# Kernel tuning notes

Hardware: AMD Instinct MI355X
Metric: run time of the kernel (lower is better)

The kernel has to match this reference:

```python
import jax, jax.numpy as jnp
import numpy as np

COMMITMENT_COST = 0.25
NUM_EMBEDDINGS = 512
EMBEDDING_DIM = 64


def setup_inputs() -> dict:
    key = jax.random.key(0)
    k1, k2 = jax.random.split(key)
    inputs = jax.random.normal(k1, (32, EMBEDDING_DIM, 64, 64), dtype=jnp.float32)  # NCHW
    embedding_weight = jax.random.normal(k2, (NUM_EMBEDDINGS, EMBEDDING_DIM), dtype=jnp.float32)
    return {"inputs": inputs, "embedding_weight": embedding_weight}


def reference(inputs, embedding_weight):
    # NCHW -> NHWC, flatten to [N, D]
    x = jnp.transpose(inputs, (0, 2, 3, 1))  # [B,H,W,D]
    input_shape = x.shape
    flat = x.reshape(-1, EMBEDDING_DIM)  # [N, D]

    distances = (jnp.sum(flat * flat, axis=1, keepdims=True)
                 + jnp.sum(embedding_weight * embedding_weight, axis=1)
                 - 2.0 * jnp.matmul(flat, embedding_weight.T))

    encoding_indices = jnp.argmin(distances, axis=1)  # [N]
    encodings = jax.nn.one_hot(encoding_indices, NUM_EMBEDDINGS, dtype=jnp.float32)  # [N, K]

    # quantized lookup (== encodings @ embedding_weight)
    quantized = jnp.take(embedding_weight, encoding_indices, axis=0).reshape(input_shape)

    # commitment loss (eval path; EMA buffer updates are a training-time side effect)
    encoder_loss = jnp.mean((jax.lax.stop_gradient(quantized) - x) ** 2)
    loss = COMMITMENT_COST * encoder_loss

    # straight-through estimator
    quantized_st = x + jax.lax.stop_gradient(quantized - x)

    avg_probs = jnp.mean(encodings, axis=0)
    perplexity = jnp.exp(-jnp.sum(avg_probs * jnp.log(avg_probs + 1e-10)))

    return (loss, jnp.transpose(quantized_st, (0, 3, 1, 2)), perplexity, encodings)
```

## Files before the change

### kernel.cpp

```cpp
#include <hip/hip_runtime.h>
#include <math.h>

#define N_ROWS 131072
#define D 64
#define K 512
#define BLK 512
#define ROWS_PER_BLK 512
#define GRID (N_ROWS / ROWS_PER_BLK)
#define MARGIN 4e-3f


typedef __attribute__((ext_vector_type(8))) _Float16 f16x8;
typedef __attribute__((ext_vector_type(4))) float    f32x4;

#define MFMA(a, b, c) __builtin_amdgcn_mfma_f32_16x16x32_f16((a), (b), (c), 0, 0, 0)

#define OFF_EH   0
#define OFF_EL   65536
#define OFF_XH   0
#define OFF_XL   65536
#define OFF_E2   131072
#define OFF_IDX  133120
#define OFF_REF  135168
#define OFF_HIST 137216
#define OFF_RED  139264
#define ARENA_SZ 143360

__global__ __launch_bounds__(256) void vq_e2_kernel(
    const float* __restrict__ emb, float* __restrict__ e2)
{
    int k = blockIdx.x * blockDim.x + threadIdx.x;
    if (k < K) {
        const float* e = emb + k * D;
        float s = 0.f;
        #pragma unroll
        for (int d = 0; d < D; ++d) s = fmaf(e[d], e[d], s);
        e2[k] = s;
    }
}

__device__ __forceinline__ unsigned pk2(_Float16 a, _Float16 b) {
    return (unsigned)__builtin_bit_cast(unsigned short, a) |
           ((unsigned)__builtin_bit_cast(unsigned short, b) << 16);
}

#define CT_ALL(M) M(0) M(1) M(2) M(3)
#define UPD(rt, s, ki) { \
    bool lt1 = (s) < s1_##rt; bool lt2 = (s) < s2_##rt; \
    s2_##rt = lt1 ? s1_##rt : (lt2 ? (s) : s2_##rt); \
    i2_##rt = lt1 ? i1_##rt : (lt2 ? (ki) : i2_##rt); \
    s1_##rt = lt1 ? (s) : s1_##rt; \
    i1_##rt = lt1 ? (ki) : i1_##rt; }

__device__ __forceinline__ void dist_pass(
    const char* ebase, const float* e2L, int fq, int fr,
    f16x8 xh0_0, f16x8 xh0_1, f16x8 xl0_0, f16x8 xl0_1,
    f16x8 xh1_0, f16x8 xh1_1, f16x8 xl1_0, f16x8 xl1_1,
    int* s_idxL, int* s_refL, int row0)
{
    float s1_0 = INFINITY, s2_0 = INFINITY, s1_1 = INFINITY, s2_1 = INFINITY;
    int   i1_0 = 0, i2_0 = 0, i1_1 = 0, i2_1 = 0;

    for (int cb = 0; cb < 8; ++cb) {
        const int cbBase = cb * 64 + fq * 4;

#define LDE2(ct) f32x4 e2q##ct = *(const f32x4*)(e2L + cb * 64 + ct * 16 + fq * 4);
        CT_ALL(LDE2)
#undef LDE2

#define LDE(ct) \
        const int c##ct = cb * 64 + ct * 16 + fr; \
        const char* rb##ct = ebase + c##ct * 128; \
        const unsigned xr##ct = (unsigned)((c##ct & 7) << 4); \
        f16x8 eh##ct##_0 = *(const f16x8*)(rb##ct + OFF_EH + (((unsigned)(fq*16 +  0)) ^ xr##ct)); \
        f16x8 eh##ct##_1 = *(const f16x8*)(rb##ct + OFF_EH + (((unsigned)(fq*16 + 64)) ^ xr##ct)); \
        f16x8 el##ct##_0 = *(const f16x8*)(rb##ct + OFF_EL + (((unsigned)(fq*16 +  0)) ^ xr##ct)); \
        f16x8 el##ct##_1 = *(const f16x8*)(rb##ct + OFF_EL + (((unsigned)(fq*16 + 64)) ^ xr##ct));
        CT_ALL(LDE)
#undef LDE

#define ACC1(rt, ct) \
        f32x4 a##rt##_##ct = {0.f, 0.f, 0.f, 0.f}; \
        a##rt##_##ct = MFMA(eh##ct##_0, xh##rt##_0, a##rt##_##ct); \
        a##rt##_##ct = MFMA(eh##ct##_1, xh##rt##_1, a##rt##_##ct); \
        a##rt##_##ct = MFMA(el##ct##_0, xh##rt##_0, a##rt##_##ct); \
        a##rt##_##ct = MFMA(el##ct##_1, xh##rt##_1, a##rt##_##ct); \
        a##rt##_##ct = MFMA(eh##ct##_0, xl##rt##_0, a##rt##_##ct); \
        a##rt##_##ct = MFMA(eh##ct##_1, xl##rt##_1, a##rt##_##ct);
#define ACC_CT(ct) ACC1(0, ct) ACC1(1, ct)
        CT_ALL(ACC_CT)
#undef ACC_CT
#undef ACC1

#define SCJ(rt, ct, j) { \
        float s = fmaf(-2.f, a##rt##_##ct[j], e2q##ct[j]); \
        int ki = cbBase + ct * 16 + j; \
        UPD(rt, s, ki) }
#define SC4(rt, ct) SCJ(rt, ct, 0) SCJ(rt, ct, 1) SCJ(rt, ct, 2) SCJ(rt, ct, 3)
#define SC_CT(ct) SC4(0, ct) SC4(1, ct)
        CT_ALL(SC_CT)
#undef SC_CT
#undef SC4
#undef SCJ
    }

#define MERGE(rt, off) { \
    float b1 = __shfl_xor(s1_##rt, off); int bi1 = __shfl_xor(i1_##rt, off); \
    float b2 = __shfl_xor(s2_##rt, off); int bi2 = __shfl_xor(i2_##rt, off); \
    bool bf = (b1 < s1_##rt) || (b1 == s1_##rt && bi1 < i1_##rt); \
    float c1 = bf ? b1 : s1_##rt; int ci1 = bf ? bi1 : i1_##rt; \
    float lw = bf ? s1_##rt : b1; int lwi = bf ? i1_##rt : bi1; \
    float d2 = bf ? b2 : s2_##rt; int di2 = bf ? bi2 : i2_##rt; \
    bool ds = (d2 < lw) || (d2 == lw && di2 < lwi); \
    s1_##rt = c1; i1_##rt = ci1; \
    s2_##rt = ds ? d2 : lw; i2_##rt = ds ? di2 : lwi; }
    MERGE(0, 16) MERGE(0, 32) MERGE(1, 16) MERGE(1, 32)
#undef MERGE

    if (fq == 0) {
        s_idxL[row0 + fr] = i1_0;
        s_refL[row0 + fr] = (s2_0 - s1_0 < MARGIN) ? i2_0 : -1;
        s_idxL[row0 + fr + 16] = i1_1;
        s_refL[row0 + fr + 16] = (s2_1 - s1_1 < MARGIN) ? i2_1 : -1;
    }
}

__global__ __launch_bounds__(BLK, 2) void vq_main_kernel(
    const float* __restrict__ in,
    const float* __restrict__ emb,
    const float* __restrict__ e2g,
    unsigned int* __restrict__ counts,
    unsigned long long* __restrict__ loss_acc,
    float* __restrict__ quant_out,
    float* __restrict__ enc_out)
{
    __shared__ __align__(16) char s_arena[ARENA_SZ];
    float*        e2L    = (float*)(s_arena + OFF_E2);
    int*          s_idxL = (int*)(s_arena + OFF_IDX);
    int*          s_refL = (int*)(s_arena + OFF_REF);
    unsigned int* s_hstL = (unsigned int*)(s_arena + OFF_HIST);
    double*       s_redL = (double*)(s_arena + OFF_RED);

    const int tid  = threadIdx.x;
    const int lane = tid & 63;
    const int w    = tid >> 6;
    const int fr   = lane & 15;
    const int fq   = lane >> 4;

    {
        const int nn = blockIdx.x * ROWS_PER_BLK + tid;
        const int bb = nn >> 12, hww = nn & 4095;
        const float* xp = in + (size_t)bb * 262144 + hww;
        char* xhW = s_arena + OFF_XH;
        char* xlW = s_arena + OFF_XL;
        #pragma unroll
        for (int i = 0; i < 64; i += 2) {
            float f0 = xp[i * 4096];
            float f1 = xp[(i + 1) * 4096];
            _Float16 h0 = (_Float16)f0; _Float16 l0 = (_Float16)(f0 - (float)h0);
            _Float16 h1 = (_Float16)f1; _Float16 l1 = (_Float16)(f1 - (float)h1);
            unsigned off = (unsigned)(tid * 64 + i) * 2u;
            *(unsigned*)(xhW + off) = pk2(h0, h1);
            *(unsigned*)(xlW + off) = pk2(l0, l1);
        }
    }
    __syncthreads();

    const _Float16* xhL = (const _Float16*)(s_arena + OFF_XH);
    const _Float16* xlL = (const _Float16*)(s_arena + OFF_XL);
    const int xr0 = w * 64 + fr;
#define LDXF(t) \
    f16x8 xh##t##_0 = *(const f16x8*)(xhL + (xr0 + t * 16) * 64 + fq * 8); \
    f16x8 xh##t##_1 = *(const f16x8*)(xhL + (xr0 + t * 16) * 64 + fq * 8 + 32); \
    f16x8 xl##t##_0 = *(const f16x8*)(xlL + (xr0 + t * 16) * 64 + fq * 8); \
    f16x8 xl##t##_1 = *(const f16x8*)(xlL + (xr0 + t * 16) * 64 + fq * 8 + 32);
    LDXF(0) LDXF(1) LDXF(2) LDXF(3)
#undef LDXF
    __syncthreads();

    {
        char* eb = s_arena;
        #pragma unroll
        for (int it = 0; it < 16; ++it) {
            int j = tid + it * 512;
            int c = j >> 4, q = j & 15;
            float4 e = ((const float4*)emb)[j];
            _Float16 h0 = (_Float16)e.x; _Float16 l0 = (_Float16)(e.x - (float)h0);
            _Float16 h1 = (_Float16)e.y; _Float16 l1 = (_Float16)(e.y - (float)h1);
            _Float16 h2 = (_Float16)e.z; _Float16 l2 = (_Float16)(e.z - (float)h2);
            _Float16 h3 = (_Float16)e.w; _Float16 l3 = (_Float16)(e.w - (float)h3);
            unsigned xr = (unsigned)((c & 7) << 4);
            unsigned base = (unsigned)(c * 128) + (((unsigned)(q * 8)) ^ xr);
            *(uint2*)(eb + OFF_EH + base) = make_uint2(pk2(h0, h1), pk2(h2, h3));
            *(uint2*)(eb + OFF_EL + base) = make_uint2(pk2(l0, l1), pk2(l2, l3));
        }
        e2L[tid] = e2g[tid];
        s_hstL[tid] = 0u;
    }
    __syncthreads();

    dist_pass(s_arena, e2L, fq, fr,
              xh0_0, xh0_1, xl0_0, xl0_1, xh1_0, xh1_1, xl1_0, xl1_1,
              s_idxL, s_refL, w * 64);
    dist_pass(s_arena, e2L, fq, fr,
              xh2_0, xh2_1, xl2_0, xl2_1, xh3_0, xh3_1, xl3_0, xl3_1,
              s_idxL, s_refL, w * 64 + 32);
    __syncthreads();

    float lsum = 0.f;
    {
        const int n = blockIdx.x * ROWS_PER_BLK + tid;
        const int b = n >> 12, hw = n & 4095;
        const float* xin = in + (size_t)b * 262144 + hw;
        int i1 = s_idxL[tid];
        const int ir = s_refL[tid];
        if (ir >= 0) {
            double dA = 0.0, dB = 0.0;
            const float* eA = emb + i1 * D;
            const float* eB = emb + ir * D;
            for (int d = 0; d < D; ++d) {
                double xv = (double)xin[d * 4096];
                double tA = xv - (double)eA[d]; dA = fma(tA, tA, dA);
                double tB = xv - (double)eB[d]; dB = fma(tB, tB, dB);
            }
            if (dB < dA || (dB == dA && ir < i1)) { i1 = ir; s_idxL[tid] = ir; }
        }
        atomicAdd(&s_hstL[i1], 1u);

        const float4* eq = (const float4*)(emb + (size_t)i1 * D);
        float* qout = quant_out + (size_t)b * 262144 + hw;
        #pragma unroll
        for (int i = 0; i < 16; ++i) {
            float4 q = eq[i];
            float x0 = xin[(4 * i + 0) * 4096], x1 = xin[(4 * i + 1) * 4096];
            float x2 = xin[(4 * i + 2) * 4096], x3 = xin[(4 * i + 3) * 4096];
            float d0 = q.x - x0; lsum = fmaf(d0, d0, lsum);
            float d1 = q.y - x1; lsum = fmaf(d1, d1, lsum);
            float d2 = q.z - x2; lsum = fmaf(d2, d2, lsum);
            float d3 = q.w - x3; lsum = fmaf(d3, d3, lsum);
            qout[(4 * i + 0) * 4096] = q.x; qout[(4 * i + 1) * 4096] = q.y;
            qout[(4 * i + 2) * 4096] = q.z; qout[(4 * i + 3) * 4096] = q.w;
        }
    }

    s_redL[tid] = (double)lsum;
    __syncthreads();
    for (int s = BLK / 2; s > 0; s >>= 1) {
        if (tid < s) s_redL[tid] += s_redL[tid + s];
        __syncthreads();
    }
    if (tid == 0) {
        unsigned long long q =
            (unsigned long long)(long long)llrint(s_redL[0] * 1073741824.0);
        atomicAdd(loss_acc, q);
    }

    {
        unsigned int c = s_hstL[tid];
        if (c) atomicAdd(&counts[tid], c);
    }

    float* enc = enc_out + (size_t)blockIdx.x * (size_t)(ROWS_PER_BLK * K);
    const int grp = tid >> 7;
    const int col4 = (tid & 127) * 4;
    for (int rr = 0; rr < ROWS_PER_BLK; rr += 4) {
        int row = rr + grp;
        int ir = s_idxL[row];
        float4 v;
        v.x = (col4 + 0 == ir) ? 1.f : 0.f;
        v.y = (col4 + 1 == ir) ? 1.f : 0.f;
        v.z = (col4 + 2 == ir) ? 1.f : 0.f;
        v.w = (col4 + 3 == ir) ? 1.f : 0.f;
        *reinterpret_cast<float4*>(enc + (size_t)row * K + col4) = v;
    }
}

__global__ __launch_bounds__(512) void vq_final_kernel(
    const unsigned int* __restrict__ counts,
    const unsigned long long* __restrict__ loss_acc,
    float* __restrict__ out_loss,
    float* __restrict__ out_perp)
{
    __shared__ double sp[512];
    int t = threadIdx.x;
    double p = (double)counts[t] / (double)N_ROWS;
    sp[t] = p * log(p + 1e-10);
    __syncthreads();
    for (int s = 256; s > 0; s >>= 1) {
        if (t < s) sp[t] += sp[t + s];
        __syncthreads();
    }
    if (t == 0) {
        double ls = (double)(long long)(*loss_acc) * (1.0 / 1073741824.0);
        *out_loss = (float)(0.25 * ls / 8388608.0);
        *out_perp = (float)exp(-sp[0]);
    }
}

extern "C" void kernel_launch(void* const* d_in, const int* in_sizes, int n_in,
                              void* d_out, int out_size, void* d_ws, size_t ws_size,
                              hipStream_t stream) {
    const float* in  = (const float*)d_in[0];
    const float* emb = (const float*)d_in[1];
    float* out = (float*)d_out;

    unsigned int* counts = (unsigned int*)d_ws;
    unsigned long long* loss_acc = (unsigned long long*)((char*)d_ws + 2048);
    float* e2 = (float*)((char*)d_ws + 4096);

    hipMemsetAsync(d_ws, 0, 2056, stream);
    vq_e2_kernel<<<2, 256, 0, stream>>>(emb, e2);
    vq_main_kernel<<<GRID, BLK, 0, stream>>>(in, emb, e2, counts, loss_acc,
                                             out + 1, out + 8388610);
    vq_final_kernel<<<1, 512, 0, stream>>>(counts, loss_acc, out, out + 8388609);
}
```

Measured before the change: 150.4 us.

## Move one-hot encoding writes to separate kernel and use nontemporal stores

The main kernel now stashes each row's chosen index as an int in the first word of its encodings row, and a new kernel expands these into full one-hot rows with wide nontemporal stores. Quantized output stores also become nontemporal. The aim is to take the 256MB encodings write out of the compute-heavy main kernel so it can run as a pure streaming kernel with better occupancy. The cost is an extra launch and a dependent read of the stashed indices from global memory, which the expanding kernel then overwrites.

```diff
diff --git a/kernel.cpp b/kernel.cpp
--- a/kernel.cpp
+++ b/kernel.cpp
@@ -8,6 +8,9 @@
 #define ROWS_PER_BLK 512
 #define GRID (N_ROWS / ROWS_PER_BLK)
 #define MARGIN 4e-3f
+#define ENC_BLK 256
+#define ENC_ROWS_PER_BLK 64
+#define ENC_GRID (N_ROWS / ENC_ROWS_PER_BLK)
 
 
 typedef __attribute__((ext_vector_type(8))) _Float16 f16x8;
@@ -223,9 +226,11 @@
                 double tA = xv - (double)eA[d]; dA = fma(tA, tA, dA);
                 double tB = xv - (double)eB[d]; dB = fma(tB, tB, dB);
             }
-            if (dB < dA || (dB == dA && ir < i1)) { i1 = ir; s_idxL[tid] = ir; }
+            if (dB < dA || (dB == dA && ir < i1)) i1 = ir;
         }
         atomicAdd(&s_hstL[i1], 1u);
+
+        *(int*)(enc_out + (size_t)n * K) = i1;
 
         const float4* eq = (const float4*)(emb + (size_t)i1 * D);
         float* qout = quant_out + (size_t)b * 262144 + hw;
@@ -238,8 +243,10 @@
             float d1 = q.y - x1; lsum = fmaf(d1, d1, lsum);
             float d2 = q.z - x2; lsum = fmaf(d2, d2, lsum);
             float d3 = q.w - x3; lsum = fmaf(d3, d3, lsum);
-            qout[(4 * i + 0) * 4096] = q.x; qout[(4 * i + 1) * 4096] = q.y;
-            qout[(4 * i + 2) * 4096] = q.z; qout[(4 * i + 3) * 4096] = q.w;
+            __builtin_nontemporal_store(q.x, &qout[(4 * i + 0) * 4096]);
+            __builtin_nontemporal_store(q.y, &qout[(4 * i + 1) * 4096]);
+            __builtin_nontemporal_store(q.z, &qout[(4 * i + 2) * 4096]);
+            __builtin_nontemporal_store(q.w, &qout[(4 * i + 3) * 4096]);
         }
     }
 
@@ -259,19 +266,37 @@
         unsigned int c = s_hstL[tid];
         if (c) atomicAdd(&counts[tid], c);
     }
-
-    float* enc = enc_out + (size_t)blockIdx.x * (size_t)(ROWS_PER_BLK * K);
-    const int grp = tid >> 7;
-    const int col4 = (tid & 127) * 4;
-    for (int rr = 0; rr < ROWS_PER_BLK; rr += 4) {
-        int row = rr + grp;
-        int ir = s_idxL[row];
-        float4 v;
-        v.x = (col4 + 0 == ir) ? 1.f : 0.f;
-        v.y = (col4 + 1 == ir) ? 1.f : 0.f;
-        v.z = (col4 + 2 == ir) ? 1.f : 0.f;
-        v.w = (col4 + 3 == ir) ? 1.f : 0.f;
-        *reinterpret_cast<float4*>(enc + (size_t)row * K + col4) = v;
+}
+
+__global__ __launch_bounds__(ENC_BLK) void vq_enc_kernel(
+    float* __restrict__ enc)
+{
+    const int tid  = threadIdx.x;
+    const int wv   = tid >> 6;
+    const int lane = tid & 63;
+    const size_t row0 = (size_t)blockIdx.x * ENC_ROWS_PER_BLK + (size_t)wv * 16;
+
+    int idxs[16];
+    #pragma unroll
+    for (int i = 0; i < 16; ++i)
+        idxs[i] = *(const int*)(enc + (row0 + i) * K);
+
+    const int c0 = lane * 8;
+    #pragma unroll
+    for (int i = 0; i < 16; ++i) {
+        const int idx = idxs[i];
+        float* rp = enc + (row0 + i) * K + c0;
+        f32x4 v0, v1;
+        v0.x = (c0 + 0 == idx) ? 1.f : 0.f;
+        v0.y = (c0 + 1 == idx) ? 1.f : 0.f;
+        v0.z = (c0 + 2 == idx) ? 1.f : 0.f;
+        v0.w = (c0 + 3 == idx) ? 1.f : 0.f;
+        v1.x = (c0 + 4 == idx) ? 1.f : 0.f;
+        v1.y = (c0 + 5 == idx) ? 1.f : 0.f;
+        v1.z = (c0 + 6 == idx) ? 1.f : 0.f;
+        v1.w = (c0 + 7 == idx) ? 1.f : 0.f;
+        __builtin_nontemporal_store(v0, (f32x4*)rp);
+        __builtin_nontemporal_store(v1, (f32x4*)(rp + 4));
     }
 }
 
@@ -312,5 +337,6 @@
     vq_e2_kernel<<<2, 256, 0, stream>>>(emb, e2);
     vq_main_kernel<<<GRID, BLK, 0, stream>>>(in, emb, e2, counts, loss_acc,
                                              out + 1, out + 8388610);
+    vq_enc_kernel<<<ENC_GRID, ENC_BLK, 0, stream>>>(out + 8388610);
     vq_final_kernel<<<1, 512, 0, stream>>>(counts, loss_acc, out, out + 8388609);
 }
```

Result: slower. 189.9 us (+26.3%).
